# Kernel optimization log

Measured on AMD Instinct MI355X. Metric: run time of the kernel, lower is better.

## Reference

```python
import jax, jax.numpy as jnp
import numpy as np

# Model constants (from init_kwargs)
N_ATOMS = 30000
N_PAIRS = 300000
NF_IN = 64
NF_OUT = 64
N_DIST = 20
MIND_SOFT = 0.85
MAXD_SOFT = 5.0
HARD_CUTOFF = 6.5


def setup_inputs() -> dict:
    key = jax.random.key(0)
    k = jax.random.split(key, 8)
    in_features = jax.random.normal(k[0], (N_ATOMS, NF_IN), dtype=jnp.float32)
    pair_first = jax.random.randint(k[1], (N_PAIRS,), 0, N_ATOMS)
    pair_second = jax.random.randint(k[2], (N_PAIRS,), 0, N_ATOMS)
    dist_pairs = jax.random.uniform(k[3], (N_PAIRS,), dtype=jnp.float32,
                                    minval=MIND_SOFT, maxval=HARD_CUTOFF)
    # InverseSensitivityModule init: mu uniformly spaced in inverse-distance space
    mu = jnp.linspace(1.0 / MAXD_SOFT, 1.0 / MIND_SOFT, N_DIST, dtype=jnp.float32)
    sigma = jnp.full((N_DIST,), (1.0 / MIND_SOFT - 1.0 / MAXD_SOFT) / N_DIST,
                     dtype=jnp.float32)
    # xavier-normal-ish init scales
    int_weights = jax.random.normal(k[4], (N_DIST, NF_OUT, NF_IN), dtype=jnp.float32) \
        * np.sqrt(2.0 / (NF_IN + NF_OUT)).astype(np.float32)
    w_self = jax.random.normal(k[5], (NF_OUT, NF_IN), dtype=jnp.float32) \
        * np.sqrt(2.0 / (NF_IN + NF_OUT)).astype(np.float32)
    b_self = jax.random.normal(k[6], (NF_OUT,), dtype=jnp.float32) * 0.01
    return {"in_features": in_features, "pair_first": pair_first,
            "pair_second": pair_second, "dist_pairs": dist_pairs,
            "mu": mu, "sigma": sigma, "int_weights": int_weights,
            "w_self": w_self, "b_self": b_self}


def _sensitivity(dist, mu, sigma):
    # Inverse-distance Gaussian sensitivities with smooth cosine hard cutoff.
    inv_d = 1.0 / dist  # [P]
    gauss = jnp.exp(-0.5 * ((inv_d[:, None] - mu[None, :]) / sigma[None, :]) ** 2)  # [P, n_dist]
    cut = jnp.cos(0.5 * jnp.pi * dist / HARD_CUTOFF) ** 2
    cut = jnp.where(dist < HARD_CUTOFF, cut, 0.0)
    return gauss * cut[:, None]


def reference(in_features, pair_first, pair_second, dist_pairs,
              mu, sigma, int_weights, w_self, b_self):
    n_atoms = in_features.shape[0]
    sense = _sensitivity(dist_pairs, mu, sigma)              # [P, n_dist]
    # envsum: env[a, nu, f] = sum_{p: pair_first[p]==a} sense[p, nu] * in_features[pair_second[p], f]
    neigh = in_features[pair_second]                          # [P, nf_in] gather
    contrib = sense[:, :, None] * neigh[:, None, :]           # [P, n_dist, nf_in]
    env = jax.ops.segment_sum(
        contrib.reshape(contrib.shape[0], N_DIST * NF_IN),
        pair_first, num_segments=n_atoms)                     # [A, n_dist*nf_in]
    # interaction matmul: weights permuted (n_dist, nf_in, nf_out) then flattened
    weights_rs = jnp.transpose(int_weights, (0, 2, 1)).reshape(N_DIST * NF_IN, NF_OUT)
    features_out = env @ weights_rs                           # [A, nf_out]
    features_out += in_features @ w_self.T + b_self           # self interaction
    return features_out
```

## Files before the change

kernel.cpp:

```cpp
#include <hip/hip_runtime.h>
#include <math.h>

#define N_ATOMS    30000
#define N_PAIRS    300000
#define CAP        48
#define NF         64
#define ND         20
#define K_ENV      1280
#define K_TOT      1344
#define NKSTEP     42
#define KSH        21
#define HARD_CUT   6.5f
#define BA         16
#define ESTRIDE    1352
#define NM1        ((unsigned)(N_ATOMS - 1))

#define INVD_LO    0.15384615385f
#define INVD_RANGE 1.02262443439f
#define QS         (65535.0f / INVD_RANGE)
#define DQ         (INVD_RANGE / 65535.0f)
#define NEXP2      (-0.7213475204444817f)

typedef short    s16x8  __attribute__((ext_vector_type(8)));
typedef __bf16   bf16x8 __attribute__((ext_vector_type(8)));
typedef unsigned u32x4  __attribute__((ext_vector_type(4)));
typedef float    f32x4  __attribute__((ext_vector_type(4)));
typedef float    f32x16 __attribute__((ext_vector_type(16)));

typedef __attribute__((address_space(1))) const void gconst_void;
typedef __attribute__((address_space(3))) void       lds_void;

__device__ __forceinline__ unsigned short f2bf(float x) {
    union { float f; unsigned u; } v; v.f = x;
    unsigned r = v.u + 0x7fffu + ((v.u >> 16) & 1u);
    return (unsigned short)(r >> 16);
}
__device__ __forceinline__ unsigned pkbf(float a, float b) {
    return (unsigned)f2bf(a) | ((unsigned)f2bf(b) << 16);
}
__device__ __forceinline__ float senseval(unsigned w0, unsigned lcb, int kidx, int cnt,
                                          float zA, float zB, bool nuok) {
    float uu = (float)(w0 & 0xffffu);
    float z  = __builtin_fmaf(uu, zA, zB);
    float ar = __builtin_fmaf(z * z, NEXP2, __uint_as_float(lcb));
    float e  = __builtin_amdgcn_exp2f(ar);
    return (nuok && kidx < cnt) ? e : 0.0f;
}

__global__ void k_prep(const float* __restrict__ iw, const float* __restrict__ wself,
                       const float* __restrict__ mu, const float* __restrict__ sigma,
                       const float* __restrict__ x,
                       unsigned short* __restrict__ WtB, int* __restrict__ cnts,
                       float2* __restrict__ msr, unsigned* __restrict__ xb16) {
    if (blockIdx.x < 42) {
        int idx = blockIdx.x * 256 + threadIdx.x;
        if (idx >= NKSTEP * 4 * 64) return;
        int l  = idx & 63;
        int q  = (idx >> 6) & 3;
        int ks = idx >> 8;
        int n  = q * 16 + (l & 15);
        int kb = ks * 32 + (l >> 4) * 8;
        u32x4 u;
        #pragma unroll
        for (int jj = 0; jj < 4; jj++) {
            unsigned short lo, hi;
            #pragma unroll
            for (int e = 0; e < 2; e++) {
                int k = kb + 2 * jj + e;
                float val;
                if (k < K_ENV) {
                    int t  = k / 640;
                    int rm = k - t * 640;
                    int g  = rm >> 7;
                    int c  = (rm & 127) >> 2;
                    int r  = k & 3;
                    int nu = 4 * g + r;
                    int f  = 2 * c + t;
                    val = iw[(nu * NF + n) * NF + f];
                } else {
                    val = wself[n * NF + (k - K_ENV)];
                }
                if (e == 0) lo = f2bf(val); else hi = f2bf(val);
            }
            u[jj] = (unsigned)lo | ((unsigned)hi << 16);
        }
        *(u32x4*)&WtB[idx * 8] = u;
    } else if (blockIdx.x < 160) {
        int i = (blockIdx.x - 42) * 256 + threadIdx.x;
        if (i < N_ATOMS) cnts[i] = 0;
    } else if (blockIdx.x == 160) {
        int i = threadIdx.x;
        if (i < ND) { float2 m; m.x = mu[i]; m.y = 1.0f / sigma[i]; msr[i] = m; }
    } else {
        int o = (blockIdx.x - 161) * 256 + threadIdx.x;
        if (o < N_ATOMS * 32 / 4) {
            int wbase = o * 4;
            const float* src = &x[(size_t)wbase * 2];
            float2 f0 = *(const float2*)(src);
            float2 f1 = *(const float2*)(src + 2);
            float2 f2 = *(const float2*)(src + 4);
            float2 f3 = *(const float2*)(src + 6);
            u32x4 u;
            u[0] = pkbf(f0.x, f0.y);
            u[1] = pkbf(f1.x, f1.y);
            u[2] = pkbf(f2.x, f2.y);
            u[3] = pkbf(f3.x, f3.y);
            *(u32x4*)&xb16[wbase] = u;
        }
    }
}

__global__ void k_scatter(const int* __restrict__ first, const int* __restrict__ second,
                          const float* __restrict__ dist, int* __restrict__ cnts,
                          uint2* __restrict__ pk) {
    int p = (blockIdx.x * 256 + threadIdx.x) * 2;
    if (p >= N_PAIRS) return;
    int2   f2 = *(const int2*)&first[p];
    int2   s2 = *(const int2*)&second[p];
    float2 d2 = *(const float2*)&dist[p];
    {
        float d    = d2.x;
        float invd = 1.0f / d;
        float tq   = fmaxf((invd - INVD_LO) * QS + 0.5f, 0.0f);
        unsigned u = min((unsigned)tq, 65535u);
        float co   = __cosf(0.2416609733530613f * d);
        float lc   = fmaxf(__log2f(co * co), -10000.0f);
        int pos = atomicAdd(&cnts[f2.x], 1);
        if (pos < CAP) {
            uint2 v; v.x = ((unsigned)s2.x << 16) | u; v.y = __float_as_uint(lc);
            pk[(size_t)f2.x * CAP + pos] = v;
        }
    }
    {
        float d    = d2.y;
        float invd = 1.0f / d;
        float tq   = fmaxf((invd - INVD_LO) * QS + 0.5f, 0.0f);
        unsigned u = min((unsigned)tq, 65535u);
        float co   = __cosf(0.2416609733530613f * d);
        float lc   = fmaxf(__log2f(co * co), -10000.0f);
        int pos = atomicAdd(&cnts[f2.y], 1);
        if (pos < CAP) {
            uint2 v; v.x = ((unsigned)s2.y << 16) | u; v.y = __float_as_uint(lc);
            pk[(size_t)f2.y * CAP + pos] = v;
        }
    }
}

__global__ void __launch_bounds__(512, 4)
k_main(const unsigned* __restrict__ xb16, const int* __restrict__ cnts,
       const uint2* __restrict__ pk, const float2* __restrict__ msr,
       const unsigned short* __restrict__ WtB, const float* __restrict__ bself,
       float* __restrict__ out) {
    __shared__ unsigned short env[BA * ESTRIDE];
    __shared__ uint2 pkl[BA * CAP];
    const int t  = threadIdx.x;
    const int w  = t >> 6;
    const int l  = t & 63;
    const int h  = l >> 5;
    const int cl = l & 31;
    const int a0 = blockIdx.x * BA;

    if (w < 6) {
        const char* gsrc = (const char*)(pk + (size_t)a0 * CAP) + (w * 64 + l) * 16;
        char* ldst = (char*)pkl + w * 1024;
        __builtin_amdgcn_global_load_lds((gconst_void*)gsrc, (lds_void*)ldst, 16, 0, 0);
    }

    float2 ms   = msr[min(cl, ND - 1)];
    const float isig = ms.y;
    const float zA   = DQ * isig;
    const float zB   = INVD_LO * isig - ms.x * isig;
    const bool  nuok = (cl < ND);
    const unsigned* xw = xb16 + cl;

    const int cntA = min(cnts[a0 + 2 * w + 0], CAP);
    const int cntB = min(cnts[a0 + 2 * w + 1], CAP);

    __syncthreads();

    #pragma unroll 1
    for (int ci = 0; ci < 2; ci++) {
        const int i = 2 * w + ci;
        const int a = a0 + i;
        const int cnt = ci ? cntB : cntA;
        const int nst = max((cnt + 15) >> 4, 1);
        const uint2* gb = &pkl[i * CAP];
        f32x16 acc0 = {0.f}, acc1 = {0.f};
        #pragma unroll 1
        for (int ks = 0; ks < nst; ks++) {
            const int k0 = ks * 16 + h * 8;
            const uint2* bp = gb + k0;
            uint4 q0 = *(const uint4*)(bp + 0);
            uint4 q1 = *(const uint4*)(bp + 2);
            uint4 q2 = *(const uint4*)(bp + 4);
            uint4 q3 = *(const uint4*)(bp + 6);
            unsigned g0 = xw[min(q0.x >> 16, NM1) * 32];
            unsigned g1 = xw[min(q0.z >> 16, NM1) * 32];
            unsigned g2 = xw[min(q1.x >> 16, NM1) * 32];
            unsigned g3 = xw[min(q1.z >> 16, NM1) * 32];
            unsigned g4 = xw[min(q2.x >> 16, NM1) * 32];
            unsigned g5 = xw[min(q2.z >> 16, NM1) * 32];
            unsigned g6 = xw[min(q3.x >> 16, NM1) * 32];
            unsigned g7 = xw[min(q3.z >> 16, NM1) * 32];
            u32x4 A, B0, B1;
            A[0] = pkbf(senseval(q0.x, q0.y, k0 + 0, cnt, zA, zB, nuok),
                        senseval(q0.z, q0.w, k0 + 1, cnt, zA, zB, nuok));
            A[1] = pkbf(senseval(q1.x, q1.y, k0 + 2, cnt, zA, zB, nuok),
                        senseval(q1.z, q1.w, k0 + 3, cnt, zA, zB, nuok));
            A[2] = pkbf(senseval(q2.x, q2.y, k0 + 4, cnt, zA, zB, nuok),
                        senseval(q2.z, q2.w, k0 + 5, cnt, zA, zB, nuok));
            A[3] = pkbf(senseval(q3.x, q3.y, k0 + 6, cnt, zA, zB, nuok),
                        senseval(q3.z, q3.w, k0 + 7, cnt, zA, zB, nuok));
            B0[0] = __builtin_amdgcn_perm(g1, g0, 0x05040100u);
            B0[1] = __builtin_amdgcn_perm(g3, g2, 0x05040100u);
            B0[2] = __builtin_amdgcn_perm(g5, g4, 0x05040100u);
            B0[3] = __builtin_amdgcn_perm(g7, g6, 0x05040100u);
            B1[0] = __builtin_amdgcn_perm(g1, g0, 0x07060302u);
            B1[1] = __builtin_amdgcn_perm(g3, g2, 0x07060302u);
            B1[2] = __builtin_amdgcn_perm(g5, g4, 0x07060302u);
            B1[3] = __builtin_amdgcn_perm(g7, g6, 0x07060302u);
            acc0 = __builtin_amdgcn_mfma_f32_32x32x16_bf16(
                       __builtin_bit_cast(bf16x8, A),
                       __builtin_bit_cast(bf16x8, B0), acc0, 0, 0, 0);
            acc1 = __builtin_amdgcn_mfma_f32_32x32x16_bf16(
                       __builtin_bit_cast(bf16x8, A),
                       __builtin_bit_cast(bf16x8, B1), acc1, 0, 0, 0);
        }
        unsigned short* er = &env[i * ESTRIDE];
        #pragma unroll
        for (int q = 0; q < 3; q++) {
            int g = 2 * q + h;
            if (g < 5) {
                uint2 v0, v1;
                v0.x = pkbf(acc0[4 * q + 0], acc0[4 * q + 1]);
                v0.y = pkbf(acc0[4 * q + 2], acc0[4 * q + 3]);
                v1.x = pkbf(acc1[4 * q + 0], acc1[4 * q + 1]);
                v1.y = pkbf(acc1[4 * q + 2], acc1[4 * q + 3]);
                *(uint2*)&er[g * 128 + cl * 4]       = v0;
                *(uint2*)&er[640 + g * 128 + cl * 4] = v1;
            }
        }
        unsigned sw = xb16[(size_t)a * 32 + (l >> 1)];
        er[K_ENV + l] = (unsigned short)(sw >> ((l & 1) * 16));
    }

    const int wq     = w & 3;
    const int ksbase = (w >> 2) * KSH;
    const unsigned short* wb = &WtB[((ksbase * 4 + wq) * 64 + l) * 8];
    s16x8 b0 = *(const s16x8*)(wb);
    s16x8 b1 = *(const s16x8*)(wb + 2048);
    s16x8 b2 = *(const s16x8*)(wb + 4096);
    s16x8 b3 = *(const s16x8*)(wb + 6144);
    float bs = (w < 4) ? bself[wq * 16 + (l & 15)] : 0.f;
    __syncthreads();

    {
        const int m16  = l & 15;
        const int quad = l >> 4;
        f32x4 acc = {0.f, 0.f, 0.f, 0.f};
        for (int kk = 0; kk < KSH; kk++) {
            int ks = ksbase + kk;
            s16x8 afrag = *(const s16x8*)&env[m16 * ESTRIDE + ks * 32 + quad * 8];
            s16x8 bcur = b0;
            b0 = b1; b1 = b2; b2 = b3;
            int nx = (kk + 4 < KSH) ? kk + 4 : KSH - 1;
            b3 = *(const s16x8*)(wb + (size_t)nx * 2048);
            acc = __builtin_amdgcn_mfma_f32_16x16x32_bf16(
                      __builtin_bit_cast(bf16x8, afrag),
                      __builtin_bit_cast(bf16x8, bcur), acc, 0, 0, 0);
        }
        float* red = (float*)pkl;
        if (w >= 4) {
            *(f32x4*)&red[((w - 4) * 64 + l) * 4] = acc;
        }
        __syncthreads();
        if (w < 4) {
            f32x4 other = *(const f32x4*)&red[(w * 64 + l) * 4];
            #pragma unroll
            for (int r = 0; r < 4; r++) {
                int row = quad * 4 + r;
                out[(size_t)(a0 + row) * NF + wq * 16 + m16] = acc[r] + other[r] + bs;
            }
        }
    }
}

extern "C" void kernel_launch(void* const* d_in, const int* in_sizes, int n_in,
                              void* d_out, int out_size, void* d_ws, size_t ws_size,
                              hipStream_t stream) {
    const float* x      = (const float*)d_in[0];
    const int*   first  = (const int*)d_in[1];
    const int*   second = (const int*)d_in[2];
    const float* dist   = (const float*)d_in[3];
    const float* mu     = (const float*)d_in[4];
    const float* sigma  = (const float*)d_in[5];
    const float* iw     = (const float*)d_in[6];
    const float* wself  = (const float*)d_in[7];
    const float* bself  = (const float*)d_in[8];
    float* out = (float*)d_out;

    char* ws = (char*)d_ws;
    unsigned short* WtB  = (unsigned short*)(ws);
    int*            cnts = (int*)(ws + 172032);
    float2*         msr  = (float2*)(ws + 292032);
    uint2*          pk   = (uint2*)(ws + 292192);
    unsigned*       xb16 = (unsigned*)(ws + 11812192);

    k_prep<<<dim3(161 + (N_ATOMS * 8 + 255) / 256), dim3(256), 0, stream>>>(
        iw, wself, mu, sigma, x, WtB, cnts, msr, xb16);
    k_scatter<<<dim3((N_PAIRS / 2 + 255) / 256), dim3(256), 0, stream>>>(
        first, second, dist, cnts, pk);
    k_main<<<dim3(N_ATOMS / BA), dim3(512), 0, stream>>>(
        xb16, cnts, pk, msr, WtB, bself, out);
}
```

Baseline: 121.9 us.

## Double atoms per block and split the output matmul K dimension four ways

The main kernel now handles 32 atoms per block with 1024 threads instead of 16 atoms with 512. Each weight fragment loaded from global memory feeds two MFMAs, one per 16-atom half, which halves weight traffic per atom. The K dimension is padded from 42 to 44 steps with zero weights and zero env columns so it splits evenly across four wave groups, whose partial sums are reduced through LDS. Bounds checks cover the partial last block. The trade-off is a much larger LDS footprint per block, likely fewer resident blocks per CU, an extra barrier and reduction stage, and a little wasted padded work.

```diff
diff --git a/kernel.cpp b/kernel.cpp
--- a/kernel.cpp
+++ b/kernel.cpp
@@ -8,12 +8,13 @@
 #define ND         20
 #define K_ENV      1280
 #define K_TOT      1344
-#define NKSTEP     42
-#define KSH        21
+#define NKS_PAD    44
+#define KQ         11
 #define HARD_CUT   6.5f
-#define BA         16
-#define ESTRIDE    1352
+#define BA         32
+#define ESTRIDE    1416
 #define NM1        ((unsigned)(N_ATOMS - 1))
+#define NB_MAIN    ((N_ATOMS + BA - 1) / BA)
 
 #define INVD_LO    0.15384615385f
 #define INVD_RANGE 1.02262443439f
@@ -52,9 +53,8 @@
                        const float* __restrict__ x,
                        unsigned short* __restrict__ WtB, int* __restrict__ cnts,
                        float2* __restrict__ msr, unsigned* __restrict__ xb16) {
-    if (blockIdx.x < 42) {
+    if (blockIdx.x < 44) {
         int idx = blockIdx.x * 256 + threadIdx.x;
-        if (idx >= NKSTEP * 4 * 64) return;
         int l  = idx & 63;
         int q  = (idx >> 6) & 3;
         int ks = idx >> 8;
@@ -77,22 +77,24 @@
                     int nu = 4 * g + r;
                     int f  = 2 * c + t;
                     val = iw[(nu * NF + n) * NF + f];
+                } else if (k < K_TOT) {
+                    val = wself[n * NF + (k - K_ENV)];
                 } else {
-                    val = wself[n * NF + (k - K_ENV)];
+                    val = 0.0f;
                 }
                 if (e == 0) lo = f2bf(val); else hi = f2bf(val);
             }
             u[jj] = (unsigned)lo | ((unsigned)hi << 16);
         }
         *(u32x4*)&WtB[idx * 8] = u;
-    } else if (blockIdx.x < 160) {
-        int i = (blockIdx.x - 42) * 256 + threadIdx.x;
+    } else if (blockIdx.x < 162) {
+        int i = (blockIdx.x - 44) * 256 + threadIdx.x;
         if (i < N_ATOMS) cnts[i] = 0;
-    } else if (blockIdx.x == 160) {
+    } else if (blockIdx.x == 162) {
         int i = threadIdx.x;
         if (i < ND) { float2 m; m.x = mu[i]; m.y = 1.0f / sigma[i]; msr[i] = m; }
     } else {
-        int o = (blockIdx.x - 161) * 256 + threadIdx.x;
+        int o = (blockIdx.x - 163) * 256 + threadIdx.x;
         if (o < N_ATOMS * 32 / 4) {
             int wbase = o * 4;
             const float* src = &x[(size_t)wbase * 2];
@@ -146,7 +148,7 @@
     }
 }
 
-__global__ void __launch_bounds__(512, 4)
+__global__ void __launch_bounds__(1024, 4)
 k_main(const unsigned* __restrict__ xb16, const int* __restrict__ cnts,
        const uint2* __restrict__ pk, const float2* __restrict__ msr,
        const unsigned short* __restrict__ WtB, const float* __restrict__ bself,
@@ -160,7 +162,7 @@
     const int cl = l & 31;
     const int a0 = blockIdx.x * BA;
 
-    if (w < 6) {
+    if (w < 12) {
         const char* gsrc = (const char*)(pk + (size_t)a0 * CAP) + (w * 64 + l) * 16;
         char* ldst = (char*)pkl + w * 1024;
         __builtin_amdgcn_global_load_lds((gconst_void*)gsrc, (lds_void*)ldst, 16, 0, 0);
@@ -173,8 +175,9 @@
     const bool  nuok = (cl < ND);
     const unsigned* xw = xb16 + cl;
 
-    const int cntA = min(cnts[a0 + 2 * w + 0], CAP);
-    const int cntB = min(cnts[a0 + 2 * w + 1], CAP);
+    const int aA = a0 + 2 * w, aB = a0 + 2 * w + 1;
+    const int cntA = (aA < N_ATOMS) ? min(cnts[aA], CAP) : 0;
+    const int cntB = (aB < N_ATOMS) ? min(cnts[aB], CAP) : 0;
 
     __syncthreads();
 
@@ -240,46 +243,66 @@
                 *(uint2*)&er[640 + g * 128 + cl * 4] = v1;
             }
         }
-        unsigned sw = xb16[(size_t)a * 32 + (l >> 1)];
+        unsigned sw = xb16[(size_t)min((unsigned)a, NM1) * 32 + (l >> 1)];
         er[K_ENV + l] = (unsigned short)(sw >> ((l & 1) * 16));
+        er[K_TOT + l] = 0;
     }
 
     const int wq     = w & 3;
-    const int ksbase = (w >> 2) * KSH;
+    const int kq     = w >> 2;
+    const int ksbase = kq * KQ;
     const unsigned short* wb = &WtB[((ksbase * 4 + wq) * 64 + l) * 8];
     s16x8 b0 = *(const s16x8*)(wb);
     s16x8 b1 = *(const s16x8*)(wb + 2048);
     s16x8 b2 = *(const s16x8*)(wb + 4096);
     s16x8 b3 = *(const s16x8*)(wb + 6144);
-    float bs = (w < 4) ? bself[wq * 16 + (l & 15)] : 0.f;
+    float bs = (kq == 0) ? bself[wq * 16 + (l & 15)] : 0.f;
     __syncthreads();
 
     {
         const int m16  = l & 15;
         const int quad = l >> 4;
-        f32x4 acc = {0.f, 0.f, 0.f, 0.f};
-        for (int kk = 0; kk < KSH; kk++) {
-            int ks = ksbase + kk;
-            s16x8 afrag = *(const s16x8*)&env[m16 * ESTRIDE + ks * 32 + quad * 8];
+        f32x4 acc0 = {0.f, 0.f, 0.f, 0.f};
+        f32x4 acc1 = {0.f, 0.f, 0.f, 0.f};
+        for (int kk = 0; kk < KQ; kk++) {
+            int ko = (ksbase + kk) * 32 + quad * 8;
+            s16x8 af0 = *(const s16x8*)&env[m16 * ESTRIDE + ko];
+            s16x8 af1 = *(const s16x8*)&env[(m16 + 16) * ESTRIDE + ko];
             s16x8 bcur = b0;
             b0 = b1; b1 = b2; b2 = b3;
-            int nx = (kk + 4 < KSH) ? kk + 4 : KSH - 1;
+            int nx = (kk + 4 < KQ) ? kk + 4 : KQ - 1;
             b3 = *(const s16x8*)(wb + (size_t)nx * 2048);
-            acc = __builtin_amdgcn_mfma_f32_16x16x32_bf16(
-                      __builtin_bit_cast(bf16x8, afrag),
-                      __builtin_bit_cast(bf16x8, bcur), acc, 0, 0, 0);
-        }
-        float* red = (float*)pkl;
-        if (w >= 4) {
-            *(f32x4*)&red[((w - 4) * 64 + l) * 4] = acc;
+            acc0 = __builtin_amdgcn_mfma_f32_16x16x32_bf16(
+                       __builtin_bit_cast(bf16x8, af0),
+                       __builtin_bit_cast(bf16x8, bcur), acc0, 0, 0, 0);
+            acc1 = __builtin_amdgcn_mfma_f32_16x16x32_bf16(
+                       __builtin_bit_cast(bf16x8, af1),
+                       __builtin_bit_cast(bf16x8, bcur), acc1, 0, 0, 0);
         }
         __syncthreads();
-        if (w < 4) {
-            f32x4 other = *(const f32x4*)&red[(w * 64 + l) * 4];
+        char* redb = (char*)env;
+        if (kq > 0) {
+            char* wr = redb + ((kq - 1) * 4 + wq) * 2048;
+            *(f32x4*)(wr + l * 16)        = acc0;
+            *(f32x4*)(wr + 1024 + l * 16) = acc1;
+        }
+        __syncthreads();
+        if (kq == 0) {
+            #pragma unroll
+            for (int j = 0; j < 3; j++) {
+                const char* rr = redb + (j * 4 + wq) * 2048;
+                acc0 += *(const f32x4*)(rr + l * 16);
+                acc1 += *(const f32x4*)(rr + 1024 + l * 16);
+            }
             #pragma unroll
             for (int r = 0; r < 4; r++) {
                 int row = quad * 4 + r;
-                out[(size_t)(a0 + row) * NF + wq * 16 + m16] = acc[r] + other[r] + bs;
+                int ar0 = a0 + row;
+                int ar1 = a0 + 16 + row;
+                if (ar0 < N_ATOMS)
+                    out[(size_t)ar0 * NF + wq * 16 + m16] = acc0[r] + bs;
+                if (ar1 < N_ATOMS)
+                    out[(size_t)ar1 * NF + wq * 16 + m16] = acc1[r] + bs;
             }
         }
     }
@@ -301,15 +324,15 @@
 
     char* ws = (char*)d_ws;
     unsigned short* WtB  = (unsigned short*)(ws);
-    int*            cnts = (int*)(ws + 172032);
-    float2*         msr  = (float2*)(ws + 292032);
-    uint2*          pk   = (uint2*)(ws + 292192);
-    unsigned*       xb16 = (unsigned*)(ws + 11812192);
-
-    k_prep<<<dim3(161 + (N_ATOMS * 8 + 255) / 256), dim3(256), 0, stream>>>(
+    int*            cnts = (int*)(ws + 180224);
+    float2*         msr  = (float2*)(ws + 300224);
+    uint2*          pk   = (uint2*)(ws + 300384);
+    unsigned*       xb16 = (unsigned*)(ws + 11820384);
+
+    k_prep<<<dim3(163 + (N_ATOMS * 8 + 255) / 256), dim3(256), 0, stream>>>(
         iw, wself, mu, sigma, x, WtB, cnts, msr, xb16);
     k_scatter<<<dim3((N_PAIRS / 2 + 255) / 256), dim3(256), 0, stream>>>(
         first, second, dist, cnts, pk);
-    k_main<<<dim3(N_ATOMS / BA), dim3(512), 0, stream>>>(
+    k_main<<<dim3(NB_MAIN), dim3(1024), 0, stream>>>(
         xb16, cnts, pk, msr, WtB, bself, out);
 }
```

Result: slower. 125.3 us (+2.8%).
